# Kernel tuning notes

Hardware: AMD Instinct MI355X
Metric: run time of the kernel (lower is better)

## Reference

```python
import jax, jax.numpy as jnp
import numpy as np
from jax import lax

FT = 48   # feature map size (hardcoded as 48*48 in the torch decode)
C = 24    # backbone output channels
HC = 96   # head_conv
HEADS = {"hm_hp": 17, "hm": 1, "hps": 34, "hp_offset": 34}
DELTA = 1.8
SCALE = 0.02083333395421505  # ~1/48, exact literal from the module


def setup_inputs() -> dict:
    key = jax.random.key(0)
    ks = iter(jax.random.split(key, 64))
    inp = {"x": jax.random.normal(next(ks), (1, C, FT, FT), dtype=jnp.float32)}
    for h, cls in HEADS.items():
        inp[h + "_dw_w"] = jax.random.normal(next(ks), (C, 1, 3, 3), jnp.float32) * 0.1
        inp[h + "_dw_b"] = jax.random.normal(next(ks), (C,), jnp.float32) * 0.01
        inp[h + "_pw1_w"] = jax.random.normal(next(ks), (HC, C, 1, 1), jnp.float32) * 0.1
        inp[h + "_pw1_b"] = jax.random.normal(next(ks), (HC,), jnp.float32) * 0.01
        inp[h + "_pw2_w"] = jax.random.normal(next(ks), (cls, HC, 1, 1), jnp.float32) * 0.1
        inp[h + "_pw2_b"] = jax.random.normal(next(ks), (cls,), jnp.float32) * 0.01
    return inp


def _conv(x, w, groups=1):
    pad = "SAME" if w.shape[-1] == 3 else "VALID"
    return lax.conv_general_dilated(x, w, (1, 1), pad, feature_group_count=groups,
                                    dimension_numbers=("NCHW", "OIHW", "NCHW"))


def _head(x, dw_w, dw_b, pw1_w, pw1_b, pw2_w, pw2_b):
    y = _conv(x, dw_w, groups=C) + dw_b[None, :, None, None]
    y = jax.nn.relu(_conv(y, pw1_w) + pw1_b[None, :, None, None])
    return _conv(y, pw2_w) + pw2_b[None, :, None, None]


def _decode(hm_hp, hm, hps, hp_off):
    # NCHW [1,c,48,48] -> HWC
    kpt_heatmap = jax.nn.sigmoid(jnp.transpose(hm_hp[0], (1, 2, 0)))            # [48,48,17]
    center = jax.nn.sigmoid(jnp.transpose(hm[0], (1, 2, 0)))[:, :, 0]           # [48,48]
    kpt_regress = jnp.transpose(hps[0], (1, 2, 0)).reshape(FT * FT, 17, 2)
    kpt_offset = jnp.transpose(hp_off[0], (1, 2, 0)).reshape(FT * FT, 17, 2)

    rng = jnp.arange(FT, dtype=jnp.float32)
    gy = rng[:, None] - FT / 2.0
    gx = rng[None, :] - FT / 2.0
    w2c = 1.0 / (jnp.sqrt(gy * gy + gx * gx) + DELTA)                            # [48,48]

    # center-weighted argmax -> single center index
    ct = jnp.argmax((center * w2c).reshape(-1))
    ct_y = (ct // FT).astype(jnp.float32)
    ct_x = (ct % FT).astype(jnp.float32)

    kpt_coor = kpt_regress[ct] + jnp.stack([ct_y, ct_x])                         # [17,2]

    # distance-weighted per-keypoint argmax over the heatmap
    dy = rng[:, None, None] - kpt_coor[:, 0]                                     # [48,1,17]
    dx = rng[None, :, None] - kpt_coor[:, 1]                                     # [1,48,17]
    dist_weight = jnp.sqrt(dy * dy + dx * dx) + DELTA                            # [48,48,17]
    scores = (kpt_heatmap / dist_weight).reshape(FT * FT, 17)
    top = jnp.argmax(scores, axis=0)                                             # [17]

    ys = (top // FT).astype(jnp.float32)
    xs = (top % FT).astype(jnp.float32)
    k17 = jnp.arange(17)
    conf = kpt_heatmap.reshape(FT * FT, 17)[top, k17]                            # [17]
    off_yx = kpt_offset[top, k17]                                                # [17,2]
    coord = (off_yx + jnp.stack([ys, xs], axis=1)) * SCALE                       # [17,2]
    return jnp.concatenate([coord, conf[:, None]], axis=1).reshape(1, 1, 17, 3)


def _forward(x,
             hm_hp_dw_w, hm_hp_dw_b, hm_hp_pw1_w, hm_hp_pw1_b, hm_hp_pw2_w, hm_hp_pw2_b,
             hm_dw_w, hm_dw_b, hm_pw1_w, hm_pw1_b, hm_pw2_w, hm_pw2_b,
             hps_dw_w, hps_dw_b, hps_pw1_w, hps_pw1_b, hps_pw2_w, hps_pw2_b,
             hp_offset_dw_w, hp_offset_dw_b, hp_offset_pw1_w, hp_offset_pw1_b, hp_offset_pw2_w, hp_offset_pw2_b):
    x = x * 0.007843137718737125 - 1.0  # module's input normalization (backbone = identity)
    hm_hp = _head(x, hm_hp_dw_w, hm_hp_dw_b, hm_hp_pw1_w, hm_hp_pw1_b, hm_hp_pw2_w, hm_hp_pw2_b)
    hm = _head(x, hm_dw_w, hm_dw_b, hm_pw1_w, hm_pw1_b, hm_pw2_w, hm_pw2_b)
    hps = _head(x, hps_dw_w, hps_dw_b, hps_pw1_w, hps_pw1_b, hps_pw2_w, hps_pw2_b)
    hp_off = _head(x, hp_offset_dw_w, hp_offset_dw_b, hp_offset_pw1_w, hp_offset_pw1_b, hp_offset_pw2_w, hp_offset_pw2_b)
    return _decode(hm_hp, hm, hps, hp_off)


def reference(x,
              hm_hp_dw_w, hm_hp_dw_b, hm_hp_pw1_w, hm_hp_pw1_b, hm_hp_pw2_w, hm_hp_pw2_b,
              hm_dw_w, hm_dw_b, hm_pw1_w, hm_pw1_b, hm_pw2_w, hm_pw2_b,
              hps_dw_w, hps_dw_b, hps_pw1_w, hps_pw1_b, hps_pw2_w, hps_pw2_b,
              hp_offset_dw_w, hp_offset_dw_b, hp_offset_pw1_w, hp_offset_pw1_b, hp_offset_pw2_w, hp_offset_pw2_b):
    return _forward(x,
                    hm_hp_dw_w, hm_hp_dw_b, hm_hp_pw1_w, hm_hp_pw1_b, hm_hp_pw2_w, hm_hp_pw2_b,
                    hm_dw_w, hm_dw_b, hm_pw1_w, hm_pw1_b, hm_pw2_w, hm_pw2_b,
                    hps_dw_w, hps_dw_b, hps_pw1_w, hps_pw1_b, hps_pw2_w, hps_pw2_b,
                    hp_offset_dw_w, hp_offset_dw_b, hp_offset_pw1_w, hp_offset_pw1_b, hp_offset_pw2_w, hp_offset_pw2_b)
```

## Files before the change

kernel.cpp:

```cpp
#include <hip/hip_runtime.h>
#include <math.h>

#define FT 48
#define NPIX (FT * FT)
#define CIN 24
#define HC 96
#define NORM_SCALE 0.007843137718737125f
#define OUT_SCALE 0.02083333395421505f
#define DELTA 1.8f

__device__ __forceinline__ float sigmoidf_(float v) { return 1.0f / (1.0f + expf(-v)); }


struct P1 {
    const float* x;
    const float* hmhp_w[6];
    const float* hm_w[6];
    float* hmhp_sig;
    float* pval;
    int*   pidx;
};

__global__ __launch_bounds__(256) void k1_heads(P1 p)
{
    __shared__ float sv[4];
    __shared__ int si[4];

    const int t = threadIdx.x;
    const int lane = t & 63;
    const int split = lane & 7;
    const int b = blockIdx.x;
    const bool is_hm = (b >= 72);
    const int lb = is_hm ? b - 72 : b;
    const int pix = lb * 32 + (t >> 3);
    const int py = pix / FT;
    const int px = pix % FT;

    const float* dw_w  = is_hm ? p.hm_w[0] : p.hmhp_w[0];
    const float* dw_b  = is_hm ? p.hm_w[1] : p.hmhp_w[1];
    const float* pw1_w = is_hm ? p.hm_w[2] : p.hmhp_w[2];
    const float* pw1_b = is_hm ? p.hm_w[3] : p.hmhp_w[3];
    const float* pw2_w = is_hm ? p.hm_w[4] : p.hmhp_w[4];
    const float* pw2_b = is_hm ? p.hm_w[5] : p.hmhp_w[5];

    float part[3];
#pragma unroll
    for (int c = 0; c < 3; ++c) {
        const int ci = split * 3 + c;
        float acc = dw_b[ci];
#pragma unroll
        for (int ky = 0; ky < 3; ++ky) {
            const int yy = py + ky - 1;
#pragma unroll
            for (int kx = 0; kx < 3; ++kx) {
                const int xx = px + kx - 1;
                float v = 0.0f;
                if (yy >= 0 && yy < FT && xx >= 0 && xx < FT)
                    v = p.x[ci * NPIX + yy * FT + xx] * NORM_SCALE - 1.0f;
                acc = fmaf(dw_w[ci * 9 + ky * 3 + kx], v, acc);
            }
        }
        part[c] = acc;
    }

    float dwv[CIN];
    const int gbase = lane & ~7;
#pragma unroll
    for (int ci = 0; ci < CIN; ++ci) {
        const float v = (ci % 3 == 0) ? part[0] : ((ci % 3 == 1) ? part[1] : part[2]);
        dwv[ci] = __shfl(v, gbase | (ci / 3), 64);
    }

    if (!is_hm) {
        float oacc[17];
#pragma unroll
        for (int k = 0; k < 17; ++k) oacc[k] = 0.0f;

#pragma unroll 4
        for (int j = 0; j < 12; ++j) {
            const int co = j * 8 + split;
            float a = pw1_b[co];
#pragma unroll
            for (int ci = 0; ci < CIN; ++ci)
                a = fmaf(pw1_w[co * CIN + ci], dwv[ci], a);
            a = fmaxf(a, 0.0f);
#pragma unroll
            for (int k = 0; k < 17; ++k)
                oacc[k] = fmaf(pw2_w[k * HC + co], a, oacc[k]);
        }
#pragma unroll
        for (int off = 1; off < 8; off <<= 1)
#pragma unroll
            for (int k = 0; k < 17; ++k)
                oacc[k] += __shfl_xor(oacc[k], off, 64);
        {
            int k = split;
            p.hmhp_sig[k * NPIX + pix] = sigmoidf_(oacc[k] + pw2_b[k]);
            k = split + 8;
            p.hmhp_sig[k * NPIX + pix] = sigmoidf_(oacc[k] + pw2_b[k]);
            if (split == 0)
                p.hmhp_sig[16 * NPIX + pix] = sigmoidf_(oacc[16] + pw2_b[16]);
        }
    } else {
        float acc1 = 0.0f;
#pragma unroll 4
        for (int j = 0; j < 12; ++j) {
            const int co = j * 8 + split;
            float a = pw1_b[co];
#pragma unroll
            for (int ci = 0; ci < CIN; ++ci)
                a = fmaf(pw1_w[co * CIN + ci], dwv[ci], a);
            a = fmaxf(a, 0.0f);
            acc1 = fmaf(pw2_w[co], a, acc1);
        }
#pragma unroll
        for (int off = 1; off < 8; off <<= 1)
            acc1 += __shfl_xor(acc1, off, 64);

        float v = -1e30f;
        int idx = pix;
        if (split == 0) {
            const float o = acc1 + pw2_b[0];
            const float gy = (float)py - 24.0f, gx = (float)px - 24.0f;
            const float w = 1.0f / (sqrtf(gy * gy + gx * gx) + DELTA);
            v = sigmoidf_(o) * w;
        }
#pragma unroll
        for (int off = 1; off < 64; off <<= 1) {
            const float v2 = __shfl_xor(v, off, 64);
            const int i2 = __shfl_xor(idx, off, 64);
            if (v2 > v || (v2 == v && i2 < idx)) { v = v2; idx = i2; }
        }
        if (lane == 0) { sv[t >> 6] = v; si[t >> 6] = idx; }
        __syncthreads();
        if (t == 0) {
            float bv = sv[0]; int bi = si[0];
#pragma unroll
            for (int w2 = 1; w2 < 4; ++w2)
                if (sv[w2] > bv || (sv[w2] == bv && si[w2] < bi)) { bv = sv[w2]; bi = si[w2]; }
            p.pval[lb] = bv;
            p.pidx[lb] = bi;
        }
    }
}


struct P2 {
    const float* x;
    const float* hps_w[6];
    const float* hpo_w[6];
    const float* hmhp_sig;
    const float* pval;
    const int*   pidx;
    float* out;
};

__device__ __forceinline__ float dw_tap(const float* __restrict__ x,
                                        const float* __restrict__ dw_w,
                                        const float* __restrict__ dw_b,
                                        int ci, int pixel)
{
    const int py = pixel / FT, px = pixel % FT;
    float acc = dw_b[ci];
#pragma unroll
    for (int ky = 0; ky < 3; ++ky) {
        const int yy = py + ky - 1;
#pragma unroll
        for (int kx = 0; kx < 3; ++kx) {
            const int xx = px + kx - 1;
            float v = 0.0f;
            if (yy >= 0 && yy < FT && xx >= 0 && xx < FT)
                v = x[ci * NPIX + yy * FT + xx] * NORM_SCALE - 1.0f;
            acc = fmaf(dw_w[ci * 9 + ky * 3 + kx], v, acc);
        }
    }
    return acc;
}

__global__ __launch_bounds__(256) void k2_decode(P2 p)
{
    __shared__ float s_red[256];
    __shared__ int s_redi[256];
    __shared__ float s_dwv[CIN];
    __shared__ float sA[HC];
    __shared__ float s_ky, s_kx;
    __shared__ int s_ct, s_top;

    const int t = threadIdx.x;
    const int k = blockIdx.x;

    if (t < 128) {
        float v = -1e30f;
        int i = 0x7fffffff;
        if (t < 72) { v = p.pval[t]; i = p.pidx[t]; }
        s_red[t] = v;
        s_redi[t] = i;
    }
    __syncthreads();
    for (int s = 64; s > 0; s >>= 1) {
        if (t < s) {
            const float v2 = s_red[t + s];
            const int i2 = s_redi[t + s];
            if (v2 > s_red[t] || (v2 == s_red[t] && i2 < s_redi[t])) {
                s_red[t] = v2;
                s_redi[t] = i2;
            }
        }
        __syncthreads();
    }
    if (t == 0) s_ct = s_redi[0];
    __syncthreads();
    const int ct = s_ct;
    const float cty = (float)(ct / FT);
    const float ctx = (float)(ct % FT);

    if (t < CIN) s_dwv[t] = dw_tap(p.x, p.hps_w[0], p.hps_w[1], t, ct);
    __syncthreads();
    if (t < HC) {
        float a = p.hps_w[3][t];
#pragma unroll
        for (int ci = 0; ci < CIN; ++ci)
            a = fmaf(p.hps_w[2][t * CIN + ci], s_dwv[ci], a);
        sA[t] = fmaxf(a, 0.0f);
    }
    __syncthreads();
    if (t < 64) {
        float vy = 0.0f, vx = 0.0f;
        for (int co = t; co < HC; co += 64) {
            const float av = sA[co];
            vy = fmaf(p.hps_w[4][(2 * k) * HC + co], av, vy);
            vx = fmaf(p.hps_w[4][(2 * k + 1) * HC + co], av, vx);
        }
#pragma unroll
        for (int off = 1; off < 64; off <<= 1) {
            vy += __shfl_xor(vy, off, 64);
            vx += __shfl_xor(vx, off, 64);
        }
        if (t == 0) {
            s_ky = vy + p.hps_w[5][2 * k] + cty;
            s_kx = vx + p.hps_w[5][2 * k + 1] + ctx;
        }
    }
    __syncthreads();
    const float kcy = s_ky, kcx = s_kx;

    float best = -1e30f;
    int bi = 0x7fffffff;
    for (int i = t; i < NPIX; i += 256) {
        const int y = i / FT, xx = i % FT;
        const float dy = (float)y - kcy, dx = (float)xx - kcx;
        const float d = sqrtf(dy * dy + dx * dx) + DELTA;
        const float v = p.hmhp_sig[k * NPIX + i] / d;
        if (v > best || (v == best && i < bi)) { best = v; bi = i; }
    }
    s_red[t] = best;
    s_redi[t] = bi;
    __syncthreads();
    for (int s = 128; s > 0; s >>= 1) {
        if (t < s) {
            const float v2 = s_red[t + s];
            const int i2 = s_redi[t + s];
            if (v2 > s_red[t] || (v2 == s_red[t] && i2 < s_redi[t])) {
                s_red[t] = v2;
                s_redi[t] = i2;
            }
        }
        __syncthreads();
    }
    if (t == 0) s_top = s_redi[0];
    __syncthreads();
    const int top = s_top;

    if (t < CIN) s_dwv[t] = dw_tap(p.x, p.hpo_w[0], p.hpo_w[1], t, top);
    __syncthreads();
    if (t < HC) {
        float a = p.hpo_w[3][t];
#pragma unroll
        for (int ci = 0; ci < CIN; ++ci)
            a = fmaf(p.hpo_w[2][t * CIN + ci], s_dwv[ci], a);
        sA[t] = fmaxf(a, 0.0f);
    }
    __syncthreads();
    if (t < 64) {
        float oy = 0.0f, ox = 0.0f;
        for (int co = t; co < HC; co += 64) {
            const float av = sA[co];
            oy = fmaf(p.hpo_w[4][(2 * k) * HC + co], av, oy);
            ox = fmaf(p.hpo_w[4][(2 * k + 1) * HC + co], av, ox);
        }
#pragma unroll
        for (int off = 1; off < 64; off <<= 1) {
            oy += __shfl_xor(oy, off, 64);
            ox += __shfl_xor(ox, off, 64);
        }
        if (t == 0) {
            const float ty = (float)(top / FT), tx = (float)(top % FT);
            p.out[k * 3 + 0] = (oy + p.hpo_w[5][2 * k] + ty) * OUT_SCALE;
            p.out[k * 3 + 1] = (ox + p.hpo_w[5][2 * k + 1] + tx) * OUT_SCALE;
            p.out[k * 3 + 2] = p.hmhp_sig[k * NPIX + top];
        }
    }
}


extern "C" void kernel_launch(void* const* d_in, const int* in_sizes, int n_in,
                              void* d_out, int out_size, void* d_ws, size_t ws_size,
                              hipStream_t stream)
{
    (void)in_sizes; (void)n_in; (void)out_size; (void)ws_size;

    float* ws = (float*)d_ws;
    float* hmhp_sig = ws;
    float* pval     = ws + 17 * NPIX;
    int*   pidx     = (int*)(ws + 17 * NPIX + 72);

    P1 p1;
    p1.x = (const float*)d_in[0];
    for (int j = 0; j < 6; ++j) p1.hmhp_w[j] = (const float*)d_in[1 + j];
    for (int j = 0; j < 6; ++j) p1.hm_w[j]   = (const float*)d_in[7 + j];
    p1.hmhp_sig = hmhp_sig;
    p1.pval = pval;
    p1.pidx = pidx;

    P2 p2;
    p2.x = (const float*)d_in[0];
    for (int j = 0; j < 6; ++j) p2.hps_w[j] = (const float*)d_in[13 + j];
    for (int j = 0; j < 6; ++j) p2.hpo_w[j] = (const float*)d_in[19 + j];
    p2.hmhp_sig = hmhp_sig;
    p2.pval = pval;
    p2.pidx = pidx;
    p2.out = (float*)d_out;

    k1_heads<<<144, 256, 0, stream>>>(p1);
    k2_decode<<<17, 256, 0, stream>>>(p2);
}
```

Before: 126.7 us.

## Fuse head and decode kernels with atomic ticket grid sync and LDS-staged weights

Merges the two launches into one kernel. The last 17 blocks to take an atomic ticket wait until all 144 producer blocks have arrived, then run the decode stage. Head weights are staged into shared memory, and pw2 is transposed there, so the pointwise loops read from LDS instead of global memory. This removes one kernel launch and the gap between launches. In exchange it adds a memset launch, a spin-wait, and a dependence on all 144 blocks being co-resident.

```diff
diff --git a/kernel.cpp b/kernel.cpp
--- a/kernel.cpp
+++ b/kernel.cpp
@@ -2,158 +2,26 @@
 #include <math.h>
 
 #define FT 48
-#define NPIX (FT * FT)
+#define NPIX 2304
 #define CIN 24
 #define HC 96
 #define NORM_SCALE 0.007843137718737125f
 #define OUT_SCALE 0.02083333395421505f
 #define DELTA 1.8f
-
-__device__ __forceinline__ float sigmoidf_(float v) { return 1.0f / (1.0f + expf(-v)); }
-
-
-struct P1 {
+#define NPROD 144
+#define NDEC 17
+
+struct PF {
     const float* x;
-    const float* hmhp_w[6];
-    const float* hm_w[6];
+    const float* w[4][6];
     float* hmhp_sig;
     float* pval;
     int*   pidx;
-};
-
-__global__ __launch_bounds__(256) void k1_heads(P1 p)
-{
-    __shared__ float sv[4];
-    __shared__ int si[4];
-
-    const int t = threadIdx.x;
-    const int lane = t & 63;
-    const int split = lane & 7;
-    const int b = blockIdx.x;
-    const bool is_hm = (b >= 72);
-    const int lb = is_hm ? b - 72 : b;
-    const int pix = lb * 32 + (t >> 3);
-    const int py = pix / FT;
-    const int px = pix % FT;
-
-    const float* dw_w  = is_hm ? p.hm_w[0] : p.hmhp_w[0];
-    const float* dw_b  = is_hm ? p.hm_w[1] : p.hmhp_w[1];
-    const float* pw1_w = is_hm ? p.hm_w[2] : p.hmhp_w[2];
-    const float* pw1_b = is_hm ? p.hm_w[3] : p.hmhp_w[3];
-    const float* pw2_w = is_hm ? p.hm_w[4] : p.hmhp_w[4];
-    const float* pw2_b = is_hm ? p.hm_w[5] : p.hmhp_w[5];
-
-    float part[3];
-#pragma unroll
-    for (int c = 0; c < 3; ++c) {
-        const int ci = split * 3 + c;
-        float acc = dw_b[ci];
-#pragma unroll
-        for (int ky = 0; ky < 3; ++ky) {
-            const int yy = py + ky - 1;
-#pragma unroll
-            for (int kx = 0; kx < 3; ++kx) {
-                const int xx = px + kx - 1;
-                float v = 0.0f;
-                if (yy >= 0 && yy < FT && xx >= 0 && xx < FT)
-                    v = p.x[ci * NPIX + yy * FT + xx] * NORM_SCALE - 1.0f;
-                acc = fmaf(dw_w[ci * 9 + ky * 3 + kx], v, acc);
-            }
-        }
-        part[c] = acc;
-    }
-
-    float dwv[CIN];
-    const int gbase = lane & ~7;
-#pragma unroll
-    for (int ci = 0; ci < CIN; ++ci) {
-        const float v = (ci % 3 == 0) ? part[0] : ((ci % 3 == 1) ? part[1] : part[2]);
-        dwv[ci] = __shfl(v, gbase | (ci / 3), 64);
-    }
-
-    if (!is_hm) {
-        float oacc[17];
-#pragma unroll
-        for (int k = 0; k < 17; ++k) oacc[k] = 0.0f;
-
-#pragma unroll 4
-        for (int j = 0; j < 12; ++j) {
-            const int co = j * 8 + split;
-            float a = pw1_b[co];
-#pragma unroll
-            for (int ci = 0; ci < CIN; ++ci)
-                a = fmaf(pw1_w[co * CIN + ci], dwv[ci], a);
-            a = fmaxf(a, 0.0f);
-#pragma unroll
-            for (int k = 0; k < 17; ++k)
-                oacc[k] = fmaf(pw2_w[k * HC + co], a, oacc[k]);
-        }
-#pragma unroll
-        for (int off = 1; off < 8; off <<= 1)
-#pragma unroll
-            for (int k = 0; k < 17; ++k)
-                oacc[k] += __shfl_xor(oacc[k], off, 64);
-        {
-            int k = split;
-            p.hmhp_sig[k * NPIX + pix] = sigmoidf_(oacc[k] + pw2_b[k]);
-            k = split + 8;
-            p.hmhp_sig[k * NPIX + pix] = sigmoidf_(oacc[k] + pw2_b[k]);
-            if (split == 0)
-                p.hmhp_sig[16 * NPIX + pix] = sigmoidf_(oacc[16] + pw2_b[16]);
-        }
-    } else {
-        float acc1 = 0.0f;
-#pragma unroll 4
-        for (int j = 0; j < 12; ++j) {
-            const int co = j * 8 + split;
-            float a = pw1_b[co];
-#pragma unroll
-            for (int ci = 0; ci < CIN; ++ci)
-                a = fmaf(pw1_w[co * CIN + ci], dwv[ci], a);
-            a = fmaxf(a, 0.0f);
-            acc1 = fmaf(pw2_w[co], a, acc1);
-        }
-#pragma unroll
-        for (int off = 1; off < 8; off <<= 1)
-            acc1 += __shfl_xor(acc1, off, 64);
-
-        float v = -1e30f;
-        int idx = pix;
-        if (split == 0) {
-            const float o = acc1 + pw2_b[0];
-            const float gy = (float)py - 24.0f, gx = (float)px - 24.0f;
-            const float w = 1.0f / (sqrtf(gy * gy + gx * gx) + DELTA);
-            v = sigmoidf_(o) * w;
-        }
-#pragma unroll
-        for (int off = 1; off < 64; off <<= 1) {
-            const float v2 = __shfl_xor(v, off, 64);
-            const int i2 = __shfl_xor(idx, off, 64);
-            if (v2 > v || (v2 == v && i2 < idx)) { v = v2; idx = i2; }
-        }
-        if (lane == 0) { sv[t >> 6] = v; si[t >> 6] = idx; }
-        __syncthreads();
-        if (t == 0) {
-            float bv = sv[0]; int bi = si[0];
-#pragma unroll
-            for (int w2 = 1; w2 < 4; ++w2)
-                if (sv[w2] > bv || (sv[w2] == bv && si[w2] < bi)) { bv = sv[w2]; bi = si[w2]; }
-            p.pval[lb] = bv;
-            p.pidx[lb] = bi;
-        }
-    }
-}
-
-
-struct P2 {
-    const float* x;
-    const float* hps_w[6];
-    const float* hpo_w[6];
-    const float* hmhp_sig;
-    const float* pval;
-    const int*   pidx;
+    int*   counter;
     float* out;
 };
+
+__device__ __forceinline__ float sigmoidf_(float v) { return 1.0f / (1.0f + expf(-v)); }
 
 __device__ __forceinline__ float dw_tap(const float* __restrict__ x,
                                         const float* __restrict__ dw_w,
@@ -177,8 +45,17 @@
     return acc;
 }
 
-__global__ __launch_bounds__(256) void k2_decode(P2 p)
+__global__ __launch_bounds__(256) void fused(PF p)
 {
+    __shared__ float s_dww[216];
+    __shared__ float s_dwb[24];
+    __shared__ float s_pw1w[HC * CIN];
+    __shared__ float s_pw1b[HC];
+    __shared__ float s_pw2t[HC * 17];
+    __shared__ float s_pw2b[17];
+    __shared__ float sv[4];
+    __shared__ int si[4];
+    __shared__ int s_ticket;
     __shared__ float s_red[256];
     __shared__ int s_redi[256];
     __shared__ float s_dwv[CIN];
@@ -187,7 +64,155 @@
     __shared__ int s_ct, s_top;
 
     const int t = threadIdx.x;
-    const int k = blockIdx.x;
+    const int b = blockIdx.x;
+    const bool is_hm = (b >= 72);
+    const int lb = is_hm ? b - 72 : b;
+    const int head = is_hm ? 1 : 0;
+
+    const float* dw_w  = p.w[head][0];
+    const float* dw_b  = p.w[head][1];
+    const float* pw1_w = p.w[head][2];
+    const float* pw1_b = p.w[head][3];
+    const float* pw2_w = p.w[head][4];
+    const float* pw2_b = p.w[head][5];
+
+    if (t < 216) s_dww[t] = dw_w[t];
+    if (t < 24) s_dwb[t] = dw_b[t];
+    for (int i = t; i < HC * CIN; i += 256) s_pw1w[i] = pw1_w[i];
+    if (t < HC) s_pw1b[t] = pw1_b[t];
+    if (!is_hm) {
+        for (int i = t; i < HC * 17; i += 256) {
+            const int co = i / 17, k = i - co * 17;
+            s_pw2t[i] = pw2_w[k * HC + co];
+        }
+        if (t < 17) s_pw2b[t] = pw2_b[t];
+    } else {
+        if (t < HC) s_pw2t[t] = pw2_w[t];
+        if (t == 0) s_pw2b[0] = pw2_b[0];
+    }
+    __syncthreads();
+
+    const int lane = t & 63;
+    const int split = lane & 7;
+    const int pix = lb * 32 + (t >> 3);
+    const int py = pix / FT;
+    const int px = pix % FT;
+
+    float part[3];
+#pragma unroll
+    for (int c = 0; c < 3; ++c) {
+        const int ci = split * 3 + c;
+        float acc = s_dwb[ci];
+#pragma unroll
+        for (int ky = 0; ky < 3; ++ky) {
+            const int yy = py + ky - 1;
+#pragma unroll
+            for (int kx = 0; kx < 3; ++kx) {
+                const int xx = px + kx - 1;
+                float v = 0.0f;
+                if (yy >= 0 && yy < FT && xx >= 0 && xx < FT)
+                    v = p.x[ci * NPIX + yy * FT + xx] * NORM_SCALE - 1.0f;
+                acc = fmaf(s_dww[ci * 9 + ky * 3 + kx], v, acc);
+            }
+        }
+        part[c] = acc;
+    }
+
+    float dwv[CIN];
+    const int gbase = lane & ~7;
+#pragma unroll
+    for (int ci = 0; ci < CIN; ++ci) {
+        const float v = (ci % 3 == 0) ? part[0] : ((ci % 3 == 1) ? part[1] : part[2]);
+        dwv[ci] = __shfl(v, gbase | (ci / 3), 64);
+    }
+
+    if (!is_hm) {
+        float oacc[17];
+#pragma unroll
+        for (int k = 0; k < 17; ++k) oacc[k] = 0.0f;
+#pragma unroll 4
+        for (int j = 0; j < 12; ++j) {
+            const int co = j * 8 + split;
+            float a = s_pw1b[co];
+#pragma unroll
+            for (int ci = 0; ci < CIN; ++ci)
+                a = fmaf(s_pw1w[co * CIN + ci], dwv[ci], a);
+            a = fmaxf(a, 0.0f);
+#pragma unroll
+            for (int k = 0; k < 17; ++k)
+                oacc[k] = fmaf(s_pw2t[co * 17 + k], a, oacc[k]);
+        }
+#pragma unroll
+        for (int off = 1; off < 8; off <<= 1)
+#pragma unroll
+            for (int k = 0; k < 17; ++k)
+                oacc[k] += __shfl_xor(oacc[k], off, 64);
+        {
+            int k = split;
+            p.hmhp_sig[k * NPIX + pix] = sigmoidf_(oacc[k] + s_pw2b[k]);
+            k = split + 8;
+            p.hmhp_sig[k * NPIX + pix] = sigmoidf_(oacc[k] + s_pw2b[k]);
+            if (split == 0)
+                p.hmhp_sig[16 * NPIX + pix] = sigmoidf_(oacc[16] + s_pw2b[16]);
+        }
+    } else {
+        float acc1 = 0.0f;
+#pragma unroll 4
+        for (int j = 0; j < 12; ++j) {
+            const int co = j * 8 + split;
+            float a = s_pw1b[co];
+#pragma unroll
+            for (int ci = 0; ci < CIN; ++ci)
+                a = fmaf(s_pw1w[co * CIN + ci], dwv[ci], a);
+            a = fmaxf(a, 0.0f);
+            acc1 = fmaf(s_pw2t[co], a, acc1);
+        }
+#pragma unroll
+        for (int off = 1; off < 8; off <<= 1)
+            acc1 += __shfl_xor(acc1, off, 64);
+
+        float v = -1e30f;
+        int idx = pix;
+        if (split == 0) {
+            const float o = acc1 + s_pw2b[0];
+            const float gy = (float)py - 24.0f, gx = (float)px - 24.0f;
+            const float w = 1.0f / (sqrtf(gy * gy + gx * gx) + DELTA);
+            v = sigmoidf_(o) * w;
+        }
+#pragma unroll
+        for (int off = 1; off < 64; off <<= 1) {
+            const float v2 = __shfl_xor(v, off, 64);
+            const int i2 = __shfl_xor(idx, off, 64);
+            if (v2 > v || (v2 == v && i2 < idx)) { v = v2; idx = i2; }
+        }
+        if (lane == 0) { sv[t >> 6] = v; si[t >> 6] = idx; }
+        __syncthreads();
+        if (t == 0) {
+            float bv = sv[0]; int bi = si[0];
+#pragma unroll
+            for (int w2 = 1; w2 < 4; ++w2)
+                if (sv[w2] > bv || (sv[w2] == bv && si[w2] < bi)) { bv = sv[w2]; bi = si[w2]; }
+            p.pval[lb] = bv;
+            p.pidx[lb] = bi;
+        }
+    }
+
+    __syncthreads();
+    if (t == 0) {
+        __threadfence();
+        s_ticket = atomicAdd(p.counter, 1);
+    }
+    __syncthreads();
+    const int ticket = s_ticket;
+    if (ticket < NPROD - NDEC) return;
+    const int k = ticket - (NPROD - NDEC);
+
+    if (t == 0) {
+        while (__hip_atomic_load(p.counter, __ATOMIC_ACQUIRE, __HIP_MEMORY_SCOPE_AGENT) < NPROD)
+            __builtin_amdgcn_s_sleep(2);
+    }
+    __syncthreads();
+    __threadfence();
 
     if (t < 128) {
         float v = -1e30f;
@@ -214,13 +239,13 @@
     const float cty = (float)(ct / FT);
     const float ctx = (float)(ct % FT);
 
-    if (t < CIN) s_dwv[t] = dw_tap(p.x, p.hps_w[0], p.hps_w[1], t, ct);
+    if (t < CIN) s_dwv[t] = dw_tap(p.x, p.w[2][0], p.w[2][1], t, ct);
     __syncthreads();
     if (t < HC) {
-        float a = p.hps_w[3][t];
+        float a = p.w[2][3][t];
 #pragma unroll
         for (int ci = 0; ci < CIN; ++ci)
-            a = fmaf(p.hps_w[2][t * CIN + ci], s_dwv[ci], a);
+            a = fmaf(p.w[2][2][t * CIN + ci], s_dwv[ci], a);
         sA[t] = fmaxf(a, 0.0f);
     }
     __syncthreads();
@@ -228,8 +253,8 @@
         float vy = 0.0f, vx = 0.0f;
         for (int co = t; co < HC; co += 64) {
             const float av = sA[co];
-            vy = fmaf(p.hps_w[4][(2 * k) * HC + co], av, vy);
-            vx = fmaf(p.hps_w[4][(2 * k + 1) * HC + co], av, vx);
+            vy = fmaf(p.w[2][4][(2 * k) * HC + co], av, vy);
+            vx = fmaf(p.w[2][4][(2 * k + 1) * HC + co], av, vx);
         }
 #pragma unroll
         for (int off = 1; off < 64; off <<= 1) {
@@ -237,8 +262,8 @@
             vx += __shfl_xor(vx, off, 64);
         }
         if (t == 0) {
-            s_ky = vy + p.hps_w[5][2 * k] + cty;
-            s_kx = vx + p.hps_w[5][2 * k + 1] + ctx;
+            s_ky = vy + p.w[2][5][2 * k] + cty;
+            s_kx = vx + p.w[2][5][2 * k + 1] + ctx;
         }
     }
     __syncthreads();
@@ -271,13 +296,13 @@
     __syncthreads();
     const int top = s_top;
 
-    if (t < CIN) s_dwv[t] = dw_tap(p.x, p.hpo_w[0], p.hpo_w[1], t, top);
+    if (t < CIN) s_dwv[t] = dw_tap(p.x, p.w[3][0], p.w[3][1], t, top);
     __syncthreads();
     if (t < HC) {
-        float a = p.hpo_w[3][t];
+        float a = p.w[3][3][t];
 #pragma unroll
         for (int ci = 0; ci < CIN; ++ci)
-            a = fmaf(p.hpo_w[2][t * CIN + ci], s_dwv[ci], a);
+            a = fmaf(p.w[3][2][t * CIN + ci], s_dwv[ci], a);
         sA[t] = fmaxf(a, 0.0f);
     }
     __syncthreads();
@@ -285,8 +310,8 @@
         float oy = 0.0f, ox = 0.0f;
         for (int co = t; co < HC; co += 64) {
             const float av = sA[co];
-            oy = fmaf(p.hpo_w[4][(2 * k) * HC + co], av, oy);
-            ox = fmaf(p.hpo_w[4][(2 * k + 1) * HC + co], av, ox);
+            oy = fmaf(p.w[3][4][(2 * k) * HC + co], av, oy);
+            ox = fmaf(p.w[3][4][(2 * k + 1) * HC + co], av, ox);
         }
 #pragma unroll
         for (int off = 1; off < 64; off <<= 1) {
@@ -295,8 +320,8 @@
         }
         if (t == 0) {
             const float ty = (float)(top / FT), tx = (float)(top % FT);
-            p.out[k * 3 + 0] = (oy + p.hpo_w[5][2 * k] + ty) * OUT_SCALE;
-            p.out[k * 3 + 1] = (ox + p.hpo_w[5][2 * k + 1] + tx) * OUT_SCALE;
+            p.out[k * 3 + 0] = (oy + p.w[3][5][2 * k] + ty) * OUT_SCALE;
+            p.out[k * 3 + 1] = (ox + p.w[3][5][2 * k + 1] + tx) * OUT_SCALE;
             p.out[k * 3 + 2] = p.hmhp_sig[k * NPIX + top];
         }
     }
@@ -313,24 +338,19 @@
     float* hmhp_sig = ws;
     float* pval     = ws + 17 * NPIX;
     int*   pidx     = (int*)(ws + 17 * NPIX + 72);
-
-    P1 p1;
-    p1.x = (const float*)d_in[0];
-    for (int j = 0; j < 6; ++j) p1.hmhp_w[j] = (const float*)d_in[1 + j];
-    for (int j = 0; j < 6; ++j) p1.hm_w[j]   = (const float*)d_in[7 + j];
-    p1.hmhp_sig = hmhp_sig;
-    p1.pval = pval;
-    p1.pidx = pidx;
-
-    P2 p2;
-    p2.x = (const float*)d_in[0];
-    for (int j = 0; j < 6; ++j) p2.hps_w[j] = (const float*)d_in[13 + j];
-    for (int j = 0; j < 6; ++j) p2.hpo_w[j] = (const float*)d_in[19 + j];
-    p2.hmhp_sig = hmhp_sig;
-    p2.pval = pval;
-    p2.pidx = pidx;
-    p2.out = (float*)d_out;
-
-    k1_heads<<<144, 256, 0, stream>>>(p1);
-    k2_decode<<<17, 256, 0, stream>>>(p2);
+    int*   counter  = (int*)(ws + 17 * NPIX + 144);
+
+    PF p;
+    p.x = (const float*)d_in[0];
+    for (int h = 0; h < 4; ++h)
+        for (int j = 0; j < 6; ++j)
+            p.w[h][j] = (const float*)d_in[1 + h * 6 + j];
+    p.hmhp_sig = hmhp_sig;
+    p.pval = pval;
+    p.pidx = pidx;
+    p.counter = counter;
+    p.out = (float*)d_out;
+
+    hipMemsetAsync(counter, 0, sizeof(int), stream);
+    fused<<<NPROD, 256, 0, stream>>>(p);
 }
```

After: 136.3 us. +7.6%, slower.
